# Optimization experiments

Measured on AMD Instinct MI355X. Metric: run time of the kernel, lower is better.

The kernel has to match this reference:

```python
import jax, jax.numpy as jnp
import numpy as np
import math

# ---- hyperparameters (from __init__) ----
S = 64.0
M = 0.45
EASY_MARGIN = False
ALPHA = 0.0
BETA = 0.0
EPS_OT = 0.1   # self.eps
NITER = 6      # self.niter
COS_M = math.cos(M)
SIN_M = math.sin(M)
TH = math.cos(math.pi - M)
MM = math.sin(math.pi - M) * M

# ---- shapes ----
B = 24
D_EMB = 512
N_CLASSES = 10000
C_CH = 256   # channels -> number of OT points per image
H = 14       # spatial -> point dim H*H = 196


def setup_inputs() -> dict:
    key = jax.random.key(0)
    k1, k2, k3, k4 = jax.random.split(key, 4)
    embeddings = jax.random.normal(k1, (B, D_EMB), dtype=jnp.float32)
    conv_features = jax.random.normal(k2, (B, C_CH, H, H), dtype=jnp.float32)
    label = jax.random.randint(k3, (B,), 0, 8)
    # nn.init.normal_(kernel, std=0.01)
    kernel = jax.random.normal(k4, (D_EMB, N_CLASSES), dtype=jnp.float32) * 0.01
    return {"embeddings": embeddings, "conv_features": conv_features,
            "kernel": kernel, "label": label, "epoch": 1}


def _cdist(x, y):
    # Euclidean pairwise distance via GEMM: x (n,d), y (m,d) -> (n,m)
    x2 = jnp.sum(x * x, axis=-1)[:, None]
    y2 = jnp.sum(y * y, axis=-1)[None, :]
    d2 = jnp.maximum(x2 + y2 - 2.0 * (x @ y.T), 0.0)
    return jnp.sqrt(d2 + 1e-12)


def _sinkhorn_dist(x, y):
    # Entropic OT distance <T, C> with uniform marginals, log-domain Sinkhorn.
    C = _cdist(x, y)                       # (n, m)
    n, m = C.shape
    log_mu = -jnp.log(jnp.float32(n))
    log_nu = -jnp.log(jnp.float32(m))
    f = jnp.zeros((n,), C.dtype)
    g = jnp.zeros((m,), C.dtype)
    for _ in range(NITER):  # fixed 6 iterations
        f = -EPS_OT * jax.nn.logsumexp((g[None, :] - C) / EPS_OT + log_nu, axis=1)
        g = -EPS_OT * jax.nn.logsumexp((f[:, None] - C) / EPS_OT + log_mu, axis=0)
    T = jnp.exp((f[:, None] + g[None, :] - C) / EPS_OT + log_mu + log_nu)
    return jnp.sum(T * C)


def reference(embeddings, conv_features, kernel, label, epoch):
    b = embeddings.shape[0]
    emb = embeddings / jnp.linalg.norm(embeddings, axis=1, keepdims=True)
    kn = kernel / jnp.linalg.norm(kernel, axis=0, keepdims=True)
    cos_theta = jnp.clip(emb @ kn, -1.0, 1.0)          # (B, n_classes)
    origin_cos = cos_theta

    rows = jnp.arange(b)
    tl = cos_theta[rows, label]                         # target logit (B,)
    sin_t = jnp.sqrt(jnp.maximum(1.0 - tl * tl, 0.0))
    ctm = tl * COS_M - sin_t * SIN_M
    if EASY_MARGIN:
        ftl = jnp.where(tl > 0.0, ctm, tl)
    else:
        ftl = jnp.where(tl > TH, ctm, tl - MM)
    cos_theta = cos_theta.at[rows, label].set(ftl)
    arcfaceloss = cos_theta * S

    # ---- triplet mining on embedding cosine similarities ----
    dists = emb @ emb.T                                 # (B, B) cosine sims
    eq = label[:, None] == label[None, :]               # (B, B) same-class mask
    # diff_low[a,p,n] = cos(a,n) - cos(a,p)
    diff = dists[:, None, :] - dists[:, :, None]        # (a, p, n)
    valid = eq[:, :, None] & (~eq)[:, None, :] & (diff > -ALPHA)
    n_cosine_pair = jnp.sum(valid)

    if epoch >= 0:
        feats = conv_features.reshape(b, conv_features.shape[1], -1)  # (B, C, H*H)
        # batched Sinkhorn distance for all (a,b) image pairs: (B, B)
        D = jax.vmap(lambda xa: jax.vmap(lambda xb: _sinkhorn_dist(xa, xb))(feats))(feats)
        dis = jnp.maximum(D[:, :, None] - D[:, None, :], -BETA)       # (a, p, n)
        hit = valid & (dis > 0.0)
        ot_pair = jnp.sum(hit)
        wass = jnp.sum(jnp.where(hit, dis, 0.0))
        wass_loss = jnp.where(wass > 0.0,
                              wass / jnp.maximum(ot_pair, 1).astype(wass.dtype),
                              jnp.zeros((), wass.dtype))
    else:
        ot_pair = jnp.zeros((), jnp.int32)
        wass_loss = jnp.zeros(())

    return (arcfaceloss, wass_loss, origin_cos * S, n_cosine_pair, ot_pair)
```

## Files before the change

### kernel.cpp

```cpp
#include <hip/hip_runtime.h>
#include <math.h>

#define B_SZ 24
#define D_EMBD 512
#define N_CLS 10000
#define CC 256
#define HH 196

#define NPAIR 276
#define NARC 40
#define NGRAM 36

#define S_SCALE 64.0f
#define COS_M 0.9004471023526769f
#define SIN_M 0.43496553411123023f
#define TH_C (-0.9004471023526769f)
#define MM_C 0.19573449035005357f
#define KSC 14.4269504088896f
#define C2E 0.0693147180559945f

typedef short bfrag8 __attribute__((ext_vector_type(8)));
typedef float facc4 __attribute__((ext_vector_type(4)));

#if __has_builtin(__builtin_amdgcn_exp2f)
#define EXP2F(x) __builtin_amdgcn_exp2f(x)
#else
#define EXP2F(x) exp2f(x)
#endif
#if __has_builtin(__builtin_amdgcn_logf)
#define LOG2F(x) __builtin_amdgcn_logf(x)
#else
#define LOG2F(x) __log2f(x)
#endif

__device__ inline unsigned short f2bf_rne(float x) {
    union { float f; unsigned u; } cv; cv.f = x;
    unsigned r = cv.u + 0x7FFFu + ((cv.u >> 16) & 1u);
    return (unsigned short)(r >> 16);
}
__device__ inline float bf2f(unsigned short h) {
    union { unsigned u; float f; } cv; cv.u = ((unsigned)h) << 16; return cv.f;
}

__global__ __launch_bounds__(1024) void k_fused(const float* __restrict__ emb,
        const float* __restrict__ conv, const float* __restrict__ kern,
        const int* __restrict__ label, float* __restrict__ dists,
        float* __restrict__ Dmat, float* __restrict__ out) {
    const int t = threadIdx.x;
    const int bid = blockIdx.x;

    __shared__ __align__(16) char smem[65536];

    if (bid >= NPAIR) {
        const int sb = bid - NPAIR;
        if (sb >= NARC) {
            const int gid = sb - NARC;
            int l = t & 63, w16 = t >> 6;
            if (gid == 0 && t < B_SZ) Dmat[t * B_SZ + t] = 0.f;
            int pid = gid * 16 + w16;
            if (pid >= B_SZ * B_SZ) return;
            int i = pid / B_SZ, j = pid - (pid / B_SZ) * B_SZ;
            float sij = 0.f, sii = 0.f, sjj = 0.f;
            #pragma unroll
            for (int u = 0; u < 8; ++u) {
                float vi = emb[i*D_EMBD + u*64 + l];
                float vj = emb[j*D_EMBD + u*64 + l];
                sij = fmaf(vi, vj, sij); sii = fmaf(vi, vi, sii); sjj = fmaf(vj, vj, sjj);
            }
            #pragma unroll
            for (int o = 1; o < 64; o <<= 1) {
                sij += __shfl_xor(sij, o, 64);
                sii += __shfl_xor(sii, o, 64);
                sjj += __shfl_xor(sjj, o, 64);
            }
            if (l == 0) dists[pid] = sij * rsqrtf(sii * sjj);
            return;
        }

        float* es = (float*)smem;
        float* inv_s = es + B_SZ * D_EMBD;
        int* lab_s = (int*)(inv_s + B_SZ);

        {
            const float4* s4 = (const float4*)emb;
            float4* d4 = (float4*)es;
            #pragma unroll
            for (int i = 0; i < 3; ++i) d4[i*1024 + t] = s4[i*1024 + t];
        }
        if (t < B_SZ) lab_s[t] = label[t];
        __syncthreads();
        {
            int l = t & 63, w = t >> 6;
            for (int r = w; r < B_SZ; r += 16) {
                float s = 0.f;
                #pragma unroll
                for (int u = 0; u < 8; ++u) { float v = es[r*D_EMBD + u*64 + l]; s = fmaf(v, v, s); }
                #pragma unroll
                for (int o = 1; o < 64; o <<= 1) s += __shfl_xor(s, o, 64);
                if (l == 0) inv_s[r] = rsqrtf(s);
            }
        }
        __syncthreads();

        const int cc = t >> 2, kc = t & 3;
        const int col = sb * 256 + cc;
        const int cL = col < N_CLS ? col : N_CLS - 1;
        float acc[B_SZ];
        #pragma unroll
        for (int r = 0; r < B_SZ; ++r) acc[r] = 0.f;
        float cn = 0.f;
        const int kb0 = kc << 7;
        for (int u = 0; u < 32; ++u) {
            const int um = (u + kc) & 31;
            const int kb = kb0 + (um << 2);
            float kv0 = kern[(kb+0)*N_CLS + cL];
            float kv1 = kern[(kb+1)*N_CLS + cL];
            float kv2 = kern[(kb+2)*N_CLS + cL];
            float kv3 = kern[(kb+3)*N_CLS + cL];
            cn = fmaf(kv0,kv0,cn); cn = fmaf(kv1,kv1,cn);
            cn = fmaf(kv2,kv2,cn); cn = fmaf(kv3,kv3,cn);
            #pragma unroll
            for (int r = 0; r < B_SZ; ++r) {
                const float4 e = *(const float4*)&es[r*D_EMBD + kb];
                acc[r] = fmaf(e.x, kv0, acc[r]);
                acc[r] = fmaf(e.y, kv1, acc[r]);
                acc[r] = fmaf(e.z, kv2, acc[r]);
                acc[r] = fmaf(e.w, kv3, acc[r]);
            }
        }
        cn += __shfl_xor(cn, 1, 64); cn += __shfl_xor(cn, 2, 64);
        #pragma unroll
        for (int r = 0; r < B_SZ; ++r) {
            acc[r] += __shfl_xor(acc[r], 1, 64);
            acc[r] += __shfl_xor(acc[r], 2, 64);
        }
        if (kc == 0 && col < N_CLS) {
            const float invk = rsqrtf(cn);
            #pragma unroll
            for (int r = 0; r < B_SZ; ++r) {
                float cosv = fminf(fmaxf(acc[r] * inv_s[r] * invk, -1.f), 1.f);
                float oc = cosv * S_SCALE;
                float af = oc;
                if (lab_s[r] == col) {
                    float tl = cosv;
                    float sint = sqrtf(fmaxf(1.f - tl*tl, 0.f));
                    float ctm = tl*COS_M - sint*SIN_M;
                    float ftl = (tl > TH_C) ? ctm : (tl - MM_C);
                    af = ftl * S_SCALE;
                }
                out[r*N_CLS + col] = af;
                out[240001 + r*N_CLS + col] = oc;
            }
        }
        return;
    }

    unsigned short* Ah = (unsigned short*)smem;
    unsigned short* Al = Ah + 8192;
    unsigned short* Bh = Al + 8192;
    unsigned short* Bl = Bh + 8192;
    float* rowred = (float*)smem;
    float* colred = rowred + 1024;
    float* rm_l   = colred + 1024;
    float* z_l    = rm_l + 256;
    float* g_l    = z_l + 256;
    float* na_s   = g_l + 256;
    float* nb_s   = na_s + 256;
    float* wredF  = nb_s + 256;
    float* wredG  = wredF + 4;
    float* wredD  = wredG + 4;

    const int w = t >> 6;
    const int wr = w >> 2, wc = w & 3;
    const int q = (t >> 4) & 3, c0 = t & 15;
    const int R0 = wr * 64, C0 = wc * 64;

    int rem = bid, a = 0;
    while (rem >= 23 - a) { rem -= 23 - a; ++a; }
    int b = a + 1 + rem;
    const float* xa = conv + a*CC*HH;
    const float* xb = conv + b*CC*HH;

    const int sn = t >> 2;
    const int sch = t & 3;

    facc4 acc[4][4];
    #pragma unroll
    for (int i = 0; i < 4; ++i)
        #pragma unroll
        for (int j = 0; j < 4; ++j) acc[i][j] = (facc4){0.f, 0.f, 0.f, 0.f};

    float pa = 0.f, pb = 0.f;

    for (int ks = 0; ks < 224; ks += 32) {
        __syncthreads();
        #pragma unroll
        for (int p = 0; p < 2; ++p) {
            int k0 = ks + sch*8;
            const float* src = (p ? xb : xa) + sn*HH + k0;
            float v[8];
            if (k0 + 8 <= HH) {
                const float4* s4 = (const float4*)src;
                float4 u0 = s4[0], u1 = s4[1];
                v[0]=u0.x; v[1]=u0.y; v[2]=u0.z; v[3]=u0.w;
                v[4]=u1.x; v[5]=u1.y; v[6]=u1.z; v[7]=u1.w;
            } else {
                #pragma unroll
                for (int j = 0; j < 8; ++j) v[j] = (k0 + j < HH) ? src[j] : 0.f;
            }
            float ps = 0.f;
            union { unsigned short s[8]; bfrag8 v8; } uh, ul;
            #pragma unroll
            for (int j = 0; j < 8; ++j) {
                ps = fmaf(v[j], v[j], ps);
                unsigned short hb = f2bf_rne(v[j]);
                uh.s[j] = hb;
                ul.s[j] = f2bf_rne(v[j] - bf2f(hb));
            }
            if (p) pb += ps; else pa += ps;
            unsigned short* dh = (p ? Bh : Ah) + sn*32 + sch*8;
            unsigned short* dl = (p ? Bl : Al) + sn*32 + sch*8;
            *(bfrag8*)dh = uh.v8;
            *(bfrag8*)dl = ul.v8;
        }
        __syncthreads();
        bfrag8 bh4[4], bl4[4];
        #pragma unroll
        for (int tj = 0; tj < 4; ++tj) {
            int col = C0 + tj*16 + c0;
            bh4[tj] = *(const bfrag8*)(Bh + col*32 + q*8);
            bl4[tj] = *(const bfrag8*)(Bl + col*32 + q*8);
        }
        #pragma unroll
        for (int ti = 0; ti < 4; ++ti) {
            int row = R0 + ti*16 + c0;
            bfrag8 ah = *(const bfrag8*)(Ah + row*32 + q*8);
            bfrag8 al = *(const bfrag8*)(Al + row*32 + q*8);
            #pragma unroll
            for (int tj = 0; tj < 4; ++tj) {
                acc[ti][tj] = __builtin_amdgcn_mfma_f32_16x16x32_bf16(ah, bh4[tj], acc[ti][tj], 0, 0, 0);
                acc[ti][tj] = __builtin_amdgcn_mfma_f32_16x16x32_bf16(ah, bl4[tj], acc[ti][tj], 0, 0, 0);
                acc[ti][tj] = __builtin_amdgcn_mfma_f32_16x16x32_bf16(al, bh4[tj], acc[ti][tj], 0, 0, 0);
            }
        }
    }
    __syncthreads();

    pa += __shfl_xor(pa, 1, 64); pa += __shfl_xor(pa, 2, 64);
    pb += __shfl_xor(pb, 1, 64); pb += __shfl_xor(pb, 2, 64);
    if (sch == 0) { na_s[sn] = pa; nb_s[sn] = pb; }
    if (t < 256) g_l[t] = 0.f;
    if (t < 4) wredG[t] = 0.f;
    __syncthreads();

    facc4 E[4][4];
    {
        float nbv[4];
        #pragma unroll
        for (int tj = 0; tj < 4; ++tj) nbv[tj] = nb_s[C0 + tj*16 + c0];
        #pragma unroll
        for (int ti = 0; ti < 4; ++ti) {
            facc4 nav = *(const facc4*)&na_s[R0 + ti*16 + q*4];
            #pragma unroll
            for (int tj = 0; tj < 4; ++tj) {
                #pragma unroll
                for (int r = 0; r < 4; ++r) {
                    float d2 = fmaxf(nav[r] + nbv[tj] - 2.f*acc[ti][tj][r], 0.f);
                    E[ti][tj][r] = KSC * sqrtf(d2 + 1e-12f);
                }
            }
        }
    }

    const int istar = ((c0&1)<<3) | ((c0&2)<<1) | ((c0&4)>>1) | ((c0&8)>>3);
    const int rowstar = R0 + (istar>>2)*16 + q*4 + (istar&3);
    const int tjstar = ((q&1)<<1) | (q>>1);
    const int colstar = C0 + tjstar*16 + c0;

    {
        float v16[16];
        #pragma unroll
        for (int ti = 0; ti < 4; ++ti)
            #pragma unroll
            for (int r = 0; r < 4; ++r)
                v16[ti*4+r] = fminf(fminf(E[ti][0][r], E[ti][1][r]),
                                    fminf(E[ti][2][r], E[ti][3][r]));
        #pragma unroll
        for (int p = 0; p < 4; ++p) {
            const int m = 1 << p, hsz = 8 >> p;
            const bool hi = (c0 >> p) & 1;
            #pragma unroll
            for (int j = 0; j < hsz; ++j) {
                float mine = hi ? v16[j+hsz] : v16[j];
                float send = hi ? v16[j] : v16[j+hsz];
                v16[j] = fminf(mine, __shfl_xor(send, m, 64));
            }
        }
        rowred[wc*256 + rowstar] = v16[0];
    }
    __syncthreads();
    if (t < 256)
        rm_l[t] = fminf(fminf(rowred[t], rowred[256+t]), fminf(rowred[512+t], rowred[768+t]));
    __syncthreads();

    #pragma unroll
    for (int ti = 0; ti < 4; ++ti) {
        facc4 rmv = *(const facc4*)&rm_l[R0 + ti*16 + q*4];
        #pragma unroll
        for (int tj = 0; tj < 4; ++tj)
            #pragma unroll
            for (int r = 0; r < 4; ++r)
                E[ti][tj][r] = EXP2F(rmv[r] - E[ti][tj][r]);
    }

    #pragma unroll 1
    for (int it = 0; it < 6; ++it) {
        float Gmax = fmaxf(fmaxf(wredG[0], wredG[1]), fmaxf(wredG[2], wredG[3]));
        float P4[4];
        #pragma unroll
        for (int tj = 0; tj < 4; ++tj) P4[tj] = EXP2F(g_l[C0 + tj*16 + c0] - Gmax);
        float v16[16];
        #pragma unroll
        for (int ti = 0; ti < 4; ++ti)
            #pragma unroll
            for (int r = 0; r < 4; ++r) {
                float s = 0.f;
                #pragma unroll
                for (int tj = 0; tj < 4; ++tj) s = fmaf(E[ti][tj][r], P4[tj], s);
                v16[ti*4+r] = s;
            }
        #pragma unroll
        for (int p = 0; p < 4; ++p) {
            const int m = 1 << p, hsz = 8 >> p;
            const bool hi = (c0 >> p) & 1;
            #pragma unroll
            for (int j = 0; j < hsz; ++j) {
                float mine = hi ? v16[j+hsz] : v16[j];
                float send = hi ? v16[j] : v16[j+hsz];
                v16[j] = mine + __shfl_xor(send, m, 64);
            }
        }
        rowred[wc*256 + rowstar] = v16[0];
        __syncthreads();
        if (t < 256) {
            float s = rowred[t] + rowred[256+t] + rowred[512+t] + rowred[768+t];
            float z = 8.f - Gmax - LOG2F(s);
            z_l[t] = z;
            float m = z;
            #pragma unroll
            for (int o = 1; o < 64; o <<= 1) m = fmaxf(m, __shfl_xor(m, o, 64));
            if ((t & 63) == 0) wredF[t >> 6] = m;
        }
        __syncthreads();
        float M = fmaxf(fmaxf(wredF[0], wredF[1]), fmaxf(wredF[2], wredF[3]));
        float Q[16];
        #pragma unroll
        for (int ti = 0; ti < 4; ++ti) {
            facc4 zv = *(const facc4*)&z_l[R0 + ti*16 + q*4];
            #pragma unroll
            for (int r = 0; r < 4; ++r) Q[ti*4+r] = EXP2F(zv[r] - M);
        }
        float w4[4];
        #pragma unroll
        for (int tj = 0; tj < 4; ++tj) {
            float s = 0.f;
            #pragma unroll
            for (int ti = 0; ti < 4; ++ti)
                #pragma unroll
                for (int r = 0; r < 4; ++r) s = fmaf(E[ti][tj][r], Q[ti*4+r], s);
            w4[tj] = s;
        }
        #pragma unroll
        for (int p = 0; p < 2; ++p) {
            const int m = 16 << p, hsz = 2 >> p;
            const bool hi = (q >> p) & 1;
            #pragma unroll
            for (int j = 0; j < hsz; ++j) {
                float mine = hi ? w4[j+hsz] : w4[j];
                float send = hi ? w4[j] : w4[j+hsz];
                w4[j] = mine + __shfl_xor(send, m, 64);
            }
        }
        colred[wr*256 + colstar] = w4[0];
        __syncthreads();
        if (t < 256) {
            float s = colred[t] + colred[256+t] + colred[512+t] + colred[768+t];
            float G = 8.f - M - LOG2F(s);
            g_l[t] = G;
            float m = G;
            #pragma unroll
            for (int o = 1; o < 64; o <<= 1) m = fmaxf(m, __shfl_xor(m, o, 64));
            if ((t & 63) == 0) wredG[t >> 6] = m;
        }
        __syncthreads();
    }

    {
        float G4[4];
        #pragma unroll
        for (int tj = 0; tj < 4; ++tj) G4[tj] = g_l[C0 + tj*16 + c0] - 16.f;
        float d = 0.f;
        #pragma unroll
        for (int ti = 0; ti < 4; ++ti) {
            facc4 zv = *(const facc4*)&z_l[R0 + ti*16 + q*4];
            facc4 rmv = *(const facc4*)&rm_l[R0 + ti*16 + q*4];
            #pragma unroll
            for (int tj = 0; tj < 4; ++tj) {
                #pragma unroll
                for (int r = 0; r < 4; ++r) {
                    float e = fmaxf(E[ti][tj][r], 1e-45f);
                    float lE = LOG2F(e);
                    float ce = rmv[r] - lE;
                    d = fmaf(EXP2F(zv[r] + G4[tj] + lE), ce, d);
                }
            }
        }
        d *= C2E;
        #pragma unroll
        for (int o = 1; o < 64; o <<= 1) d += __shfl_xor(d, o, 64);
        if ((t & 63) == 0) wredD[w] = d;
        __syncthreads();
        if (t == 0) {
            float s = 0.f;
            #pragma unroll
            for (int i = 0; i < 16; ++i) s += wredD[i];
            Dmat[a*B_SZ + b] = s;
            Dmat[b*B_SZ + a] = s;
        }
    }
}

__global__ __launch_bounds__(256) void k_fin(const int* __restrict__ label,
        const float* __restrict__ dists, const float* __restrict__ Dmat,
        float* __restrict__ out) {
    const int t = threadIdx.x;
    __shared__ float ds[576], Dm[576];
    __shared__ int lab[B_SZ];
    __shared__ float wls[4]; __shared__ int wnp[4], wot[4];
    for (int i = t; i < 576; i += 256) { ds[i] = dists[i]; Dm[i] = Dmat[i]; }
    if (t < B_SZ) lab[t] = label[t];
    __syncthreads();
    int np = 0, ot = 0; float wsum = 0.f;
    for (int idx = t; idx < 24*24*24; idx += 256) {
        int a2 = idx / 576;
        int rest = idx - a2*576;
        int p2 = rest / 24;
        int n2 = rest - p2*24;
        int la = lab[a2];
        if (la == lab[p2] && la != lab[n2]) {
            float diff = ds[a2*24 + n2] - ds[a2*24 + p2];
            if (diff > 0.f) {
                ++np;
                float dd = Dm[a2*24 + p2] - Dm[a2*24 + n2];
                if (dd > 0.f) { ++ot; wsum += dd; }
            }
        }
    }
    #pragma unroll
    for (int o = 1; o < 64; o <<= 1) {
        np += __shfl_xor(np, o, 64);
        ot += __shfl_xor(ot, o, 64);
        wsum += __shfl_xor(wsum, o, 64);
    }
    int w = t >> 6;
    if ((t & 63) == 0) { wnp[w] = np; wot[w] = ot; wls[w] = wsum; }
    __syncthreads();
    if (t == 0) {
        int tnp = wnp[0]+wnp[1]+wnp[2]+wnp[3];
        int tot = wot[0]+wot[1]+wot[2]+wot[3];
        float tws = wls[0]+wls[1]+wls[2]+wls[3];
        int den = tot > 1 ? tot : 1;
        float wl = (tws > 0.f) ? tws / (float)den : 0.f;
        out[240000] = wl;
        out[480001] = (float)tnp;
        out[480002] = (float)tot;
    }
}

extern "C" void kernel_launch(void* const* d_in, const int* in_sizes, int n_in,
                              void* d_out, int out_size, void* d_ws, size_t ws_size,
                              hipStream_t stream) {
    (void)in_sizes; (void)n_in; (void)out_size; (void)ws_size;
    const float* emb  = (const float*)d_in[0];
    const float* conv = (const float*)d_in[1];
    const float* kern = (const float*)d_in[2];
    const int*   lab  = (const int*)d_in[3];
    float* out = (float*)d_out;
    float* ws  = (float*)d_ws;
    float* dists = ws;
    float* Dmat  = ws + 576;

    k_fused<<<NPAIR + NARC + NGRAM, 1024, 0, stream>>>(emb, conv, kern, lab, dists, Dmat, out);
    k_fin<<<1, 256, 0, stream>>>(lab, dists, Dmat, out);
}
```

Baseline: 198.6 us.

## Double-buffer GEMM staging, cheaper bf16 split, precompute Sinkhorn row exponents

Shared memory is doubled so the next K-slice of the conv features is converted and staged while MFMAs run on the current slice, which removes one barrier per iteration. The hi/lo bf16 split now uses truncation and byte permutes in place of round-to-nearest. The row exponent q is computed once per row by 256 threads instead of by every thread, using the previous iteration's max. The final transport sum replaces a per-element exp with products of precomputed exponentials. Risks are the larger LDS footprint (128KB) and slightly different rounding in the split and in the shift term.

```diff
diff --git a/kernel.cpp b/kernel.cpp
--- a/kernel.cpp
+++ b/kernel.cpp
@@ -33,15 +33,6 @@
 #define LOG2F(x) __log2f(x)
 #endif
 
-__device__ inline unsigned short f2bf_rne(float x) {
-    union { float f; unsigned u; } cv; cv.f = x;
-    unsigned r = cv.u + 0x7FFFu + ((cv.u >> 16) & 1u);
-    return (unsigned short)(r >> 16);
-}
-__device__ inline float bf2f(unsigned short h) {
-    union { unsigned u; float f; } cv; cv.u = ((unsigned)h) << 16; return cv.f;
-}
-
 __global__ __launch_bounds__(1024) void k_fused(const float* __restrict__ emb,
         const float* __restrict__ conv, const float* __restrict__ kern,
         const int* __restrict__ label, float* __restrict__ dists,
@@ -49,7 +40,7 @@
     const int t = threadIdx.x;
     const int bid = blockIdx.x;
 
-    __shared__ __align__(16) char smem[65536];
+    __shared__ __align__(16) char smem[131072];
 
     if (bid >= NPAIR) {
         const int sb = bid - NPAIR;
@@ -155,16 +146,14 @@
         return;
     }
 
-    unsigned short* Ah = (unsigned short*)smem;
-    unsigned short* Al = Ah + 8192;
-    unsigned short* Bh = Al + 8192;
-    unsigned short* Bl = Bh + 8192;
+    unsigned short* SB = (unsigned short*)smem;
     float* rowred = (float*)smem;
     float* colred = rowred + 1024;
     float* rm_l   = colred + 1024;
     float* z_l    = rm_l + 256;
     float* g_l    = z_l + 256;
-    float* na_s   = g_l + 256;
+    float* q_l    = g_l + 256;
+    float* na_s   = q_l + 256;
     float* nb_s   = na_s + 256;
     float* wredF  = nb_s + 256;
     float* wredG  = wredF + 4;
@@ -192,11 +181,11 @@
 
     float pa = 0.f, pb = 0.f;
 
-    for (int ks = 0; ks < 224; ks += 32) {
-        __syncthreads();
+    auto stage = [&](int set, int ks) {
+        unsigned short* base = SB + set * 32768;
         #pragma unroll
         for (int p = 0; p < 2; ++p) {
-            int k0 = ks + sch*8;
+            const int k0 = ks + sch*8;
             const float* src = (p ? xb : xa) + sn*HH + k0;
             float v[8];
             if (k0 + 8 <= HH) {
@@ -209,21 +198,36 @@
                 for (int j = 0; j < 8; ++j) v[j] = (k0 + j < HH) ? src[j] : 0.f;
             }
             float ps = 0.f;
-            union { unsigned short s[8]; bfrag8 v8; } uh, ul;
-            #pragma unroll
-            for (int j = 0; j < 8; ++j) {
-                ps = fmaf(v[j], v[j], ps);
-                unsigned short hb = f2bf_rne(v[j]);
-                uh.s[j] = hb;
-                ul.s[j] = f2bf_rne(v[j] - bf2f(hb));
+            unsigned hw[4], lw[4];
+            #pragma unroll
+            for (int j = 0; j < 4; ++j) {
+                float v0 = v[2*j], v1 = v[2*j+1];
+                ps = fmaf(v0, v0, ps); ps = fmaf(v1, v1, ps);
+                unsigned u0 = __float_as_uint(v0), u1 = __float_as_uint(v1);
+                float h0 = __uint_as_float(u0 & 0xFFFF0000u);
+                float h1 = __uint_as_float(u1 & 0xFFFF0000u);
+                unsigned l0 = __float_as_uint(v0 - h0);
+                unsigned l1 = __float_as_uint(v1 - h1);
+                hw[j] = __builtin_amdgcn_perm(u1, u0, 0x07060302u);
+                lw[j] = __builtin_amdgcn_perm(l1, l0, 0x07060302u);
             }
             if (p) pb += ps; else pa += ps;
-            unsigned short* dh = (p ? Bh : Ah) + sn*32 + sch*8;
-            unsigned short* dl = (p ? Bl : Al) + sn*32 + sch*8;
-            *(bfrag8*)dh = uh.v8;
-            *(bfrag8*)dl = ul.v8;
-        }
-        __syncthreads();
+            unsigned short* dh = base + (p ? 2 : 0)*8192 + sn*32 + sch*8;
+            unsigned short* dl = base + (p ? 3 : 1)*8192 + sn*32 + sch*8;
+            *(uint4*)dh = (uint4){hw[0], hw[1], hw[2], hw[3]};
+            *(uint4*)dl = (uint4){lw[0], lw[1], lw[2], lw[3]};
+        }
+    };
+
+    stage(0, 0);
+    __syncthreads();
+    int cur = 0;
+    for (int ks = 0; ks < 224; ks += 32) {
+        if (ks + 32 < 224) stage(cur ^ 1, ks + 32);
+        unsigned short* Ah = SB + cur*32768;
+        unsigned short* Al = Ah + 8192;
+        unsigned short* Bh = Al + 8192;
+        unsigned short* Bl = Bh + 8192;
         bfrag8 bh4[4], bl4[4];
         #pragma unroll
         for (int tj = 0; tj < 4; ++tj) {
@@ -243,14 +247,15 @@
                 acc[ti][tj] = __builtin_amdgcn_mfma_f32_16x16x32_bf16(al, bh4[tj], acc[ti][tj], 0, 0, 0);
             }
         }
-    }
-    __syncthreads();
+        __syncthreads();
+        cur ^= 1;
+    }
 
     pa += __shfl_xor(pa, 1, 64); pa += __shfl_xor(pa, 2, 64);
     pb += __shfl_xor(pb, 1, 64); pb += __shfl_xor(pb, 2, 64);
     if (sch == 0) { na_s[sn] = pa; nb_s[sn] = pb; }
     if (t < 256) g_l[t] = 0.f;
-    if (t < 4) wredG[t] = 0.f;
+    if (t < 4) { wredG[t] = 0.f; wredF[t] = 8.f; }
     __syncthreads();
 
     facc4 E[4][4];
@@ -316,6 +321,7 @@
     #pragma unroll 1
     for (int it = 0; it < 6; ++it) {
         float Gmax = fmaxf(fmaxf(wredG[0], wredG[1]), fmaxf(wredG[2], wredG[3]));
+        float MS   = fmaxf(fmaxf(wredF[0], wredF[1]), fmaxf(wredF[2], wredF[3]));
         float P4[4];
         #pragma unroll
         for (int tj = 0; tj < 4; ++tj) P4[tj] = EXP2F(g_l[C0 + tj*16 + c0] - Gmax);
@@ -346,19 +352,19 @@
             float s = rowred[t] + rowred[256+t] + rowred[512+t] + rowred[768+t];
             float z = 8.f - Gmax - LOG2F(s);
             z_l[t] = z;
+            q_l[t] = EXP2F(z - MS);
             float m = z;
             #pragma unroll
             for (int o = 1; o < 64; o <<= 1) m = fmaxf(m, __shfl_xor(m, o, 64));
             if ((t & 63) == 0) wredF[t >> 6] = m;
         }
         __syncthreads();
-        float M = fmaxf(fmaxf(wredF[0], wredF[1]), fmaxf(wredF[2], wredF[3]));
         float Q[16];
         #pragma unroll
         for (int ti = 0; ti < 4; ++ti) {
-            facc4 zv = *(const facc4*)&z_l[R0 + ti*16 + q*4];
-            #pragma unroll
-            for (int r = 0; r < 4; ++r) Q[ti*4+r] = EXP2F(zv[r] - M);
+            facc4 qv = *(const facc4*)&q_l[R0 + ti*16 + q*4];
+            #pragma unroll
+            for (int r = 0; r < 4; ++r) Q[ti*4+r] = qv[r];
         }
         float w4[4];
         #pragma unroll
@@ -385,7 +391,7 @@
         __syncthreads();
         if (t < 256) {
             float s = colred[t] + colred[256+t] + colred[512+t] + colred[768+t];
-            float G = 8.f - M - LOG2F(s);
+            float G = 8.f - MS - LOG2F(s);
             g_l[t] = G;
             float m = G;
             #pragma unroll
@@ -396,22 +402,24 @@
     }
 
     {
-        float G4[4];
-        #pragma unroll
-        for (int tj = 0; tj < 4; ++tj) G4[tj] = g_l[C0 + tj*16 + c0] - 16.f;
+        float gc[4];
+        #pragma unroll
+        for (int tj = 0; tj < 4; ++tj) gc[tj] = EXP2F(g_l[C0 + tj*16 + c0] - 8.f);
         float d = 0.f;
         #pragma unroll
         for (int ti = 0; ti < 4; ++ti) {
             facc4 zv = *(const facc4*)&z_l[R0 + ti*16 + q*4];
             facc4 rmv = *(const facc4*)&rm_l[R0 + ti*16 + q*4];
+            float fr[4];
+            #pragma unroll
+            for (int r = 0; r < 4; ++r) fr[r] = EXP2F(zv[r] - 8.f);
             #pragma unroll
             for (int tj = 0; tj < 4; ++tj) {
                 #pragma unroll
                 for (int r = 0; r < 4; ++r) {
                     float e = fmaxf(E[ti][tj][r], 1e-45f);
                     float lE = LOG2F(e);
-                    float ce = rmv[r] - lE;
-                    d = fmaf(EXP2F(zv[r] + G4[tj] + lE), ce, d);
+                    d = fmaf(e * (fr[r] * gc[tj]), rmv[r] - lE, d);
                 }
             }
         }
```

Measured after the change: 247.9 us. 1.25x slower.
